# Kernel optimization log

Hardware: AMD Instinct MI355X
Metric: run time of the kernel (lower is better)

The kernel has to match this reference:

```python
import jax, jax.numpy as jnp
import numpy as np

EPS = 0.05  # mesh.epsilon boundary band


def _pool_one(adj, image, vs, edges):
    # adj: [N,N] bool, image: [N,F] f32, vs: [N,2] f32 in [0,1], edges: [2,E] int32
    N, F = image.shape
    E = edges.shape[1]
    K = N // 2                      # out_target
    tgt_kills = N - K               # number of vertices removed
    v0, v1 = edges[0], edges[1]
    # heap key = sum of squares of concat(image[v0], image[v1])
    cost = jnp.sum(image[v0] * image[v0], -1) + jnp.sum(image[v1] * image[v1], -1)
    def bnd(p):
        return (p[:, 0] < EPS) | (p[:, 0] > 1 - EPS) | (p[:, 1] < EPS) | (p[:, 1] > 1 - EPS)
    ok = ~(bnd(vs[v0]) | bnd(vs[v1]))   # boundary_mask = ~is_boundary
    # heappop of [value, id] lists == stable sort by cost (ties broken by edge id)
    order = jnp.argsort(cost)
    # sequential greedy collapse: kill v1 if edge interior and both endpoints alive
    def step(carry, eid):
        mask, nk = carry
        a, b = v0[eid], v1[eid]
        acc = ok[eid] & mask[a] & mask[b] & (nk < tgt_kills)
        mask = mask.at[b].set(mask[b] & ~acc)
        return (mask, nk + acc.astype(jnp.int32)), acc
    (mask, _), accepts = jax.lax.scan(step, (jnp.ones(N, bool), jnp.int32(0)), order)
    sv0, sv1 = v0[order], v1[order]
    # mapping m: dead vertex -> absorbing vertex (identity elsewhere)
    dead = jnp.where(accepts, sv1, N)          # N = out-of-range -> dropped
    m = jnp.arange(N).at[dead].set(sv0, mode='drop')
    # update_matrix: scatter-add collapsed vertex features into absorber rows
    upd = jnp.zeros_like(image).at[jnp.where(accepts, sv0, N)].add(image[sv1], mode='drop')
    image2 = image + upd
    # merge_vertex on adjacency: union rows then columns of merged vertices
    A = adj.astype(jnp.uint8)
    A1 = jnp.zeros_like(A).at[m].max(A)        # merge rows
    A2 = jnp.zeros_like(A1).at[m].max(A1.T).T  # merge cols
    alive = jnp.nonzero(mask, size=K, fill_value=0)[0]  # exactly K survivors
    adj_out = A2[alive][:, alive].astype(bool) & ~jnp.eye(K, dtype=bool)
    return adj_out, image2[alive]


def setup_inputs() -> dict:
    key = jax.random.key(0)
    k1, k2, k3, k4, k5 = jax.random.split(key, 5)
    B, N, F, E = 4, 8192, 64, 65536
    adj = jax.random.bernoulli(k1, 0.002, (B, N, N))
    image = jax.random.normal(k2, (B, N, F), jnp.float32)
    vs = jax.random.uniform(k3, (B, N, 2), dtype=jnp.float32)
    a = jax.random.randint(k4, (B, 1, E), 0, N)
    off = jax.random.randint(k5, (B, 1, E), 1, N)
    b = (a + off) % N                           # guarantee v0 != v1
    edges = jnp.concatenate([a, b], axis=1).astype(jnp.int32)
    return {"adj": adj, "image": image, "vs": vs, "edges": edges}


def reference(adj, image, vs, edges):
    # returns (pooled adjacency [B,N//2,N//2] bool, pooled features [B,N//2,F])
    return jax.vmap(_pool_one)(adj, image, vs, edges)
```

## Files before the change

kernel.cpp:

```cpp
#include <hip/hip_runtime.h>
#include <stdint.h>

typedef unsigned long long u64;
typedef unsigned int u32;
typedef unsigned char u8;

#define Bn 4
#define Nv 8192
#define Fd 64
#define Ed 65536
#define Kv 4096
#define TGTK 4096
#define NW 256
#define SC 8192

#define WS_FLAGS   ((size_t)0)
#define WS_ACCCNT  ((size_t)256)
#define WS_OUTBITS ((size_t)512)
#define OUTBITS_BYTES ((size_t)Bn*Kv*128*4)
#define WS_ZERO_BYTES (WS_OUTBITS + OUTBITS_BYTES)
#define WS_KEYS    (WS_ZERO_BYTES)
#define WS_SQ      (WS_KEYS + (size_t)Bn*Ed*8)
#define WS_BND     (WS_SQ + (size_t)Bn*Nv*4)
#define WS_OK      (WS_BND + (size_t)Bn*Nv)
#define WS_MAP     (WS_OK + (size_t)Bn*Ed)
#define WS_POS     (WS_MAP + (size_t)Bn*Nv*4)
#define WS_PM      (WS_POS + (size_t)Bn*Nv*4)
#define WS_ALIVEW  (WS_PM + (size_t)Bn*Nv*4)
#define WS_ALIST   (WS_ALIVEW + (size_t)Bn*NW*4)
#define WS_ACC     (WS_ALIST + (size_t)Bn*Kv*4)

__global__ void k_detect(const u8* adj, u32* flags) {
    int tid = blockIdx.x * blockDim.x + threadIdx.x;
    const u32* w = (const u32*)adj;
    bool f0 = false, f1 = false, f2 = false, f3 = false;
    for (int i = tid; i < (1 << 19); i += gridDim.x * blockDim.x) {
        u32 v = w[i];
        f0 |= (v & 0x000000FFu) != 0;
        f1 |= (v & 0x0000FF00u) != 0;
        f2 |= (v & 0x00FF0000u) != 0;
        f3 |= (v & 0xFF000000u) != 0;
    }
    u32 m = 0;
    if (__ballot(f0)) m |= 1;
    if (__ballot(f1)) m |= 2;
    if (__ballot(f2)) m |= 4;
    if (__ballot(f3)) m |= 8;
    if ((threadIdx.x & 63) == 0 && m) atomicOr(flags, m);
}

__global__ void k_vertex(const float* image, const float* vs, float* sq, u8* bnd, int* map) {
#pragma clang fp contract(off)
    int idx = blockIdx.x * 256 + threadIdx.x;
    if (idx >= Bn * Nv) return;
    const float* row = image + (size_t)idx * Fd;
    float r[8];
#pragma unroll
    for (int j = 0; j < 8; ++j) r[j] = row[j] * row[j];
#pragma unroll
    for (int i = 8; i < 64; i += 8)
#pragma unroll
        for (int j = 0; j < 8; ++j) r[j] += row[i + j] * row[i + j];
    float s = ((r[0] + r[1]) + (r[2] + r[3])) + ((r[4] + r[5]) + (r[6] + r[7]));
    sq[idx] = s;
    float x = vs[(size_t)idx * 2], y = vs[(size_t)idx * 2 + 1];
    const float LO = 0.05f;
    const float HI = (float)(1.0 - 0.05);
    bnd[idx] = ((x < LO) || (x > HI) || (y < LO) || (y > HI)) ? 1 : 0;
    map[idx] = idx & (Nv - 1);
}

__global__ void k_edge(const int* edges, const float* sq, const u8* bnd, u64* keys, u8* ok) {
    int idx = blockIdx.x * 256 + threadIdx.x;
    if (idx >= Bn * Ed) return;
    int b = idx >> 16, e = idx & (Ed - 1);
    int v0 = edges[(size_t)b * 2 * Ed + e];
    int v1 = edges[(size_t)b * 2 * Ed + Ed + e];
    float c = sq[b * Nv + v0] + sq[b * Nv + v1];
    u32 cb = __float_as_uint(c);
    keys[idx] = ((u64)cb << 16) | (u32)e;
    ok[idx] = (!bnd[b * Nv + v0] && !bnd[b * Nv + v1]) ? 1 : 0;
}

__device__ __forceinline__ void bitonic_cas(u64* s, int i, int pa, bool asc) {
    u64 a = s[i], c = s[pa];
    if ((a > c) == asc) { s[i] = c; s[pa] = a; }
}

__global__ __launch_bounds__(1024) void k_sortA(u64* keys) {
    __shared__ u64 s[SC];
    int b = blockIdx.x >> 3, ch = blockIdx.x & 7;
    u64* base = keys + (size_t)b * Ed + (size_t)ch * SC;
    int gb = ch * SC;
    for (int p = 0; p < SC / 1024; ++p) s[p * 1024 + threadIdx.x] = base[p * 1024 + threadIdx.x];
    __syncthreads();
    for (int k = 2; k <= SC; k <<= 1) {
        for (int j = k >> 1; j > 0; j >>= 1) {
            for (int p = 0; p < SC / 2048; ++p) {
                int t = p * 1024 + threadIdx.x;
                int i = ((t & ~(j - 1)) << 1) | (t & (j - 1));
                bool asc = (((gb + i) & k) == 0);
                bitonic_cas(s, i, i | j, asc);
            }
            __syncthreads();
        }
    }
    for (int p = 0; p < SC / 1024; ++p) base[p * 1024 + threadIdx.x] = s[p * 1024 + threadIdx.x];
}

__global__ void k_sortB(u64* keys, int k, int j) {
    int idx = blockIdx.x * 256 + threadIdx.x;
    if (idx >= Bn * Ed / 2) return;
    int b = idx >> 15, t = idx & (Ed / 2 - 1);
    int i = ((t & ~(j - 1)) << 1) | (t & (j - 1));
    int pa = i | j;
    bool asc = ((i & k) == 0);
    u64* base = keys + (size_t)b * Ed;
    u64 a = base[i], c = base[pa];
    if ((a > c) == asc) { base[i] = c; base[pa] = a; }
}

__global__ __launch_bounds__(1024) void k_sortC(u64* keys, int k) {
    __shared__ u64 s[SC];
    int b = blockIdx.x >> 3, ch = blockIdx.x & 7;
    u64* base = keys + (size_t)b * Ed + (size_t)ch * SC;
    int gb = ch * SC;
    for (int p = 0; p < SC / 1024; ++p) s[p * 1024 + threadIdx.x] = base[p * 1024 + threadIdx.x];
    __syncthreads();
    bool asc = ((gb & k) == 0);
    for (int j = SC / 2; j > 0; j >>= 1) {
        for (int p = 0; p < SC / 2048; ++p) {
            int t = p * 1024 + threadIdx.x;
            int i = ((t & ~(j - 1)) << 1) | (t & (j - 1));
            bitonic_cas(s, i, i | j, asc);
        }
        __syncthreads();
    }
    for (int p = 0; p < SC / 1024; ++p) base[p * 1024 + threadIdx.x] = s[p * 1024 + threadIdx.x];
}

__global__ __launch_bounds__(64) void k_greedy(const u64* keys, const int* edges, const u8* ok,
                                               int* map, u32* aliveW, int* accList, u32* accCnt) {
    int b = blockIdx.x;
    int lane = threadIdx.x;
    __shared__ u32 alive[NW];
    __shared__ u32 mlane[Nv];
    for (int i = lane; i < NW; i += 64) alive[i] = 0xFFFFFFFFu;
    for (int i = lane; i < Nv; i += 64) mlane[i] = 64u;
    __syncthreads();
    const u64* kb = keys + (size_t)b * Ed;
    const int* e0 = edges + (size_t)b * 2 * Ed;
    const int* e1 = e0 + Ed;
    const u8* okb = ok + (size_t)b * Ed;
    int nk = 0;
    for (int g = 0; g < Ed / 64 && nk < TGTK; ++g) {
        u64 key = kb[g * 64 + lane];
        int id = (int)(key & 0xFFFFu);
        int v0 = e0[id], v1 = e1[id];
        bool okk = okb[id] != 0;
        bool a0 = (alive[v0 >> 5] >> (v0 & 31)) & 1u;
        bool a1 = (alive[v1 >> 5] >> (v1 & 31)) & 1u;
        bool spec = okk && a0 && a1;
        if (spec) atomicMin(&mlane[v1], (u32)lane);
        __syncthreads();
        bool conf = false;
        if (spec) conf = (mlane[v0] < (u32)lane) || (mlane[v1] < (u32)lane);
        u64 specM = __ballot(spec);
        u64 confM = __ballot(conf);
        u64 accM = specM & ~confM;
        u64 rem = confM;
        while (rem) {
            int l = __ffsll((unsigned long long)rem) - 1;
            rem &= rem - 1;
            int bv0 = __shfl(v0, l);
            int bv1 = __shfl(v1, l);
            bool killer = ((accM >> lane) & 1ull) && (lane < l) && (v1 == bv0 || v1 == bv1);
            if (__ballot(killer) == 0ull) accM |= 1ull << l;
        }
        int cnt = __popcll(accM);
        int remK = TGTK - nk;
        bool acc = (accM >> lane) & 1ull;
        if (cnt > remK) {
            int r = __popcll(accM & ((1ull << lane) - 1ull));
            if (acc && r >= remK) acc = false;
            accM = __ballot(acc);
            cnt = remK;
        }
        if (acc) {
            atomicAnd(&alive[v1 >> 5], ~(1u << (v1 & 31)));
            map[(size_t)b * Nv + v1] = v0;
            int r = __popcll(accM & ((1ull << lane) - 1ull));
            int slot = nk + r;
            accList[((size_t)b * TGTK + slot) * 2] = v0;
            accList[((size_t)b * TGTK + slot) * 2 + 1] = v1;
        }
        if (spec) mlane[v1] = 64u;
        nk += cnt;
        __syncthreads();
    }
    for (int i = lane; i < NW; i += 64) aliveW[b * NW + i] = alive[i];
    if (lane == 0) accCnt[b] = (u32)nk;
}

__global__ __launch_bounds__(256) void k_scan(const u32* aliveW, const int* map,
                                              int* pos, int* pm, int* alist) {
    int b = blockIdx.x, tid = threadIdx.x;
    __shared__ u32 cnt[256];
    __shared__ u32 off[256];
    u32 w = aliveW[b * NW + tid];
    cnt[tid] = __popc(w);
    __syncthreads();
    if (tid == 0) { u32 s = 0; for (int i = 0; i < 256; ++i) { off[i] = s; s += cnt[i]; } }
    __syncthreads();
    u32 base = off[tid];
    int* posb = pos + (size_t)b * Nv;
    int* alb = alist + (size_t)b * Kv;
    for (int bit = 0; bit < 32; ++bit) {
        int v = tid * 32 + bit;
        int p = -1;
        if ((w >> bit) & 1u) {
            if (base < Kv) { p = (int)base; alb[base] = v; }
            base++;
        }
        posb[v] = p;
    }
    __syncthreads();
    const int* mapb = map + (size_t)b * Nv;
    int* pmb = pm + (size_t)b * Nv;
    for (int v = tid; v < Nv; v += 256) pmb[v] = posb[mapb[v]];
}

__global__ void k_fcopy(const float* image, const int* alist, float* outF) {
    int idx = blockIdx.x * 256 + threadIdx.x;
    if (idx >= Bn * Kv * 16) return;
    int b = idx >> 16, r = idx & 65535;
    int x = r >> 4, f4 = r & 15;
    int src = alist[b * Kv + x];
    const float4* s = (const float4*)(image + ((size_t)(b * Nv + src)) * Fd) + f4;
    float4* d = (float4*)(outF + ((size_t)(b * Kv + x)) * Fd) + f4;
    *d = *s;
}

__global__ __launch_bounds__(64) void k_fscat(const float* image, const int* accList,
                                              const u32* accCnt, const int* pos, float* outF) {
    int b = blockIdx.x >> 12, e = blockIdx.x & 4095;
    if (e >= (int)accCnt[b]) return;
    int v0 = accList[((size_t)b * TGTK + e) * 2];
    int v1 = accList[((size_t)b * TGTK + e) * 2 + 1];
    int x = pos[(size_t)b * Nv + v0];
    if (x < 0) return;
    int f = threadIdx.x;
    atomicAdd(outF + ((size_t)(b * Kv + x)) * Fd + f,
              image[((size_t)(b * Nv + v1)) * Fd + f]);
}

__global__ __launch_bounds__(256) void k_merge(const u8* adj, const u32* flags,
                                               const int* pm, u32* outbits) {
    int bi = blockIdx.x;
    int b = bi >> 13, i = bi & (Nv - 1);
    int t = pm[(size_t)b * Nv + i];
    if (t < 0) return;
    __shared__ u32 bits[Kv / 32];
    int tid = threadIdx.x;
    if (tid < 128) bits[tid] = 0;
    __syncthreads();
    const int* pmb = pm + (size_t)b * Nv;
    u32 fw = flags[0];
    bool bytefmt = (fw & 1) && (fw & 8);
    auto put = [&](int col) {
        int c = pmb[col];
        if (c >= 0) atomicOr(&bits[c >> 5], 1u << (c & 31));
    };
    if (bytefmt) {
        const uint4* row = (const uint4*)(adj + ((size_t)b * Nv + i) * Nv);
#pragma unroll
        for (int it = 0; it < 2; ++it) {
            uint4 v = row[it * 256 + tid];
            if (v.x | v.y | v.z | v.w) {
                int cb = (it * 256 + tid) * 16;
                u32 wv[4] = { v.x, v.y, v.z, v.w };
                for (int q = 0; q < 4; ++q) {
                    u32 u = wv[q];
                    if (!u) continue;
#pragma unroll
                    for (int kk = 0; kk < 4; ++kk)
                        if ((u >> (8 * kk)) & 0xFFu) put(cb + q * 4 + kk);
                }
            }
        }
    } else {
        const uint4* row = (const uint4*)((const u32*)adj + ((size_t)b * Nv + i) * Nv);
        for (int it = 0; it < 8; ++it) {
            uint4 v = row[it * 256 + tid];
            int cb = (it * 256 + tid) * 4;
            if (v.x) put(cb);
            if (v.y) put(cb + 1);
            if (v.z) put(cb + 2);
            if (v.w) put(cb + 3);
        }
    }
    __syncthreads();
    if (tid < 128) {
        u32 bw = bits[tid];
        if (bw) atomicOr(&outbits[((size_t)b * Kv + t) * 128 + tid], bw);
    }
}

__global__ void k_expand(const u32* outbits, float* out) {
    int idx = blockIdx.x;
    int tid = threadIdx.x;
    int b = idx >> 14, r = idx & 16383;
    int x = r >> 2, seg = r & 3;
    int c0 = seg * 1024 + tid * 4;
    u32 w = outbits[((size_t)b * Kv + x) * 128 + (c0 >> 5)];
    u32 nib = (w >> (c0 & 31)) & 0xFu;
    float4 f;
    f.x = (nib & 1) ? 1.f : 0.f;
    f.y = (nib & 2) ? 1.f : 0.f;
    f.z = (nib & 4) ? 1.f : 0.f;
    f.w = (nib & 8) ? 1.f : 0.f;
    if (x >= c0 && x < c0 + 4) ((float*)&f)[x - c0] = 0.f;
    *((float4*)(out + ((size_t)(b * Kv + x)) * Kv + c0)) = f;
}

extern "C" void kernel_launch(void* const* d_in, const int* in_sizes, int n_in,
                              void* d_out, int out_size, void* d_ws, size_t ws_size,
                              hipStream_t stream) {
    const u8* adj = (const u8*)d_in[0];
    const float* image = (const float*)d_in[1];
    const float* vs = (const float*)d_in[2];
    const int* edges = (const int*)d_in[3];
    char* ws = (char*)d_ws;
    u32* flags = (u32*)(ws + WS_FLAGS);
    u32* accCnt = (u32*)(ws + WS_ACCCNT);
    u32* outbits = (u32*)(ws + WS_OUTBITS);
    u64* keys = (u64*)(ws + WS_KEYS);
    float* sq = (float*)(ws + WS_SQ);
    u8* bnd = (u8*)(ws + WS_BND);
    u8* ok = (u8*)(ws + WS_OK);
    int* map = (int*)(ws + WS_MAP);
    int* pos = (int*)(ws + WS_POS);
    int* pm = (int*)(ws + WS_PM);
    u32* aliveW = (u32*)(ws + WS_ALIVEW);
    int* alist = (int*)(ws + WS_ALIST);
    int* accList = (int*)(ws + WS_ACC);
    float* outA = (float*)d_out;
    float* outF = outA + (size_t)Bn * Kv * Kv;

    hipMemsetAsync(d_ws, 0, WS_ZERO_BYTES, stream);
    k_detect<<<64, 256, 0, stream>>>(adj, flags);
    k_vertex<<<Bn * Nv / 256, 256, 0, stream>>>(image, vs, sq, bnd, map);
    k_edge<<<Bn * Ed / 256, 256, 0, stream>>>(edges, sq, bnd, keys, ok);
    k_sortA<<<Bn * 8, 1024, 0, stream>>>(keys);
    k_sortB<<<Bn * Ed / 2 / 256, 256, 0, stream>>>(keys, 16384, 8192);
    k_sortC<<<Bn * 8, 1024, 0, stream>>>(keys, 16384);
    k_sortB<<<Bn * Ed / 2 / 256, 256, 0, stream>>>(keys, 32768, 16384);
    k_sortB<<<Bn * Ed / 2 / 256, 256, 0, stream>>>(keys, 32768, 8192);
    k_sortC<<<Bn * 8, 1024, 0, stream>>>(keys, 32768);
    k_sortB<<<Bn * Ed / 2 / 256, 256, 0, stream>>>(keys, 65536, 32768);
    k_sortB<<<Bn * Ed / 2 / 256, 256, 0, stream>>>(keys, 65536, 16384);
    k_sortB<<<Bn * Ed / 2 / 256, 256, 0, stream>>>(keys, 65536, 8192);
    k_sortC<<<Bn * 8, 1024, 0, stream>>>(keys, 65536);
    k_greedy<<<Bn, 64, 0, stream>>>(keys, edges, ok, map, aliveW, accList, accCnt);
    k_scan<<<Bn, 256, 0, stream>>>(aliveW, map, pos, pm, alist);
    k_fcopy<<<Bn * Kv * 16 / 256, 256, 0, stream>>>(image, alist, outF);
    k_fscat<<<Bn * TGTK, 64, 0, stream>>>(image, accList, accCnt, pos, outF);
    k_merge<<<Bn * Nv, 256, 0, stream>>>(adj, flags, pm, outbits);
    k_expand<<<Bn * Kv * 4, 256, 0, stream>>>(outbits, outA);
}
```

Baseline: 2.091 ms.

## Pack edge data into sorted array and do small bitonic stages in registers

Edge endpoints and the interior flag are packed into one 32-bit word per edge, and a parallel gather kernel reorders these by sorted key. The serial greedy loop then reads one coalesced word per lane, with the next group prefetched, in place of a chain of dependent loads (key, then edges, then the ok flag). The bitonic sort kernels also handle the last three merge steps (strides 4, 2, 1) on eight elements held in registers per thread, which removes shared-memory passes and barriers. This costs one extra gather launch and two workspace buffers.

```diff
diff --git a/kernel.cpp b/kernel.cpp
--- a/kernel.cpp
+++ b/kernel.cpp
@@ -22,13 +22,14 @@
 #define WS_KEYS    (WS_ZERO_BYTES)
 #define WS_SQ      (WS_KEYS + (size_t)Bn*Ed*8)
 #define WS_BND     (WS_SQ + (size_t)Bn*Nv*4)
-#define WS_OK      (WS_BND + (size_t)Bn*Nv)
-#define WS_MAP     (WS_OK + (size_t)Bn*Ed)
+#define WS_MAP     (WS_BND + (size_t)Bn*Nv)
 #define WS_POS     (WS_MAP + (size_t)Bn*Nv*4)
 #define WS_PM      (WS_POS + (size_t)Bn*Nv*4)
 #define WS_ALIVEW  (WS_PM + (size_t)Bn*Nv*4)
 #define WS_ALIST   (WS_ALIVEW + (size_t)Bn*NW*4)
 #define WS_ACC     (WS_ALIST + (size_t)Bn*Kv*4)
+#define WS_PACK    (WS_ACC + (size_t)Bn*TGTK*2*4)
+#define WS_SPACK   (WS_PACK + (size_t)Bn*Ed*4)
 
 __global__ void k_detect(const u8* adj, u32* flags) {
     int tid = blockIdx.x * blockDim.x + threadIdx.x;
@@ -70,21 +71,24 @@
     map[idx] = idx & (Nv - 1);
 }
 
-__global__ void k_edge(const int* edges, const float* sq, const u8* bnd, u64* keys, u8* ok) {
+__global__ void k_edge(const int* edges, const float* sq, const u8* bnd, u64* keys, u32* pack) {
     int idx = blockIdx.x * 256 + threadIdx.x;
     if (idx >= Bn * Ed) return;
     int b = idx >> 16, e = idx & (Ed - 1);
     int v0 = edges[(size_t)b * 2 * Ed + e];
     int v1 = edges[(size_t)b * 2 * Ed + Ed + e];
     float c = sq[b * Nv + v0] + sq[b * Nv + v1];
-    u32 cb = __float_as_uint(c);
-    keys[idx] = ((u64)cb << 16) | (u32)e;
-    ok[idx] = (!bnd[b * Nv + v0] && !bnd[b * Nv + v1]) ? 1 : 0;
+    keys[idx] = ((u64)__float_as_uint(c) << 16) | (u32)e;
+    u32 okk = (!bnd[b * Nv + v0] && !bnd[b * Nv + v1]) ? 1u : 0u;
+    pack[idx] = (u32)v0 | ((u32)v1 << 13) | (okk << 26);
 }
 
 __device__ __forceinline__ void bitonic_cas(u64* s, int i, int pa, bool asc) {
     u64 a = s[i], c = s[pa];
     if ((a > c) == asc) { s[i] = c; s[pa] = a; }
+}
+__device__ __forceinline__ void cex(u64& a, u64& b, bool asc) {
+    if ((a > b) == asc) { u64 t = a; a = b; b = t; }
 }
 
 __global__ __launch_bounds__(1024) void k_sortA(u64* keys) {
@@ -92,10 +96,25 @@
     int b = blockIdx.x >> 3, ch = blockIdx.x & 7;
     u64* base = keys + (size_t)b * Ed + (size_t)ch * SC;
     int gb = ch * SC;
-    for (int p = 0; p < SC / 1024; ++p) s[p * 1024 + threadIdx.x] = base[p * 1024 + threadIdx.x];
-    __syncthreads();
-    for (int k = 2; k <= SC; k <<= 1) {
-        for (int j = k >> 1; j > 0; j >>= 1) {
+    int t8 = threadIdx.x * 8;
+    u64 r[8];
+#pragma unroll
+    for (int u = 0; u < 8; ++u) r[u] = base[t8 + u];
+    cex(r[0], r[1], true); cex(r[2], r[3], false); cex(r[4], r[5], true); cex(r[6], r[7], false);
+    cex(r[0], r[2], true); cex(r[1], r[3], true); cex(r[4], r[6], false); cex(r[5], r[7], false);
+    cex(r[0], r[1], true); cex(r[2], r[3], true); cex(r[4], r[5], false); cex(r[6], r[7], false);
+    {
+        bool a8 = (((gb + t8) & 8) == 0);
+        cex(r[0], r[4], a8); cex(r[1], r[5], a8); cex(r[2], r[6], a8); cex(r[3], r[7], a8);
+        cex(r[0], r[2], a8); cex(r[1], r[3], a8); cex(r[4], r[6], a8); cex(r[5], r[7], a8);
+        cex(r[0], r[1], a8); cex(r[2], r[3], a8); cex(r[4], r[5], a8); cex(r[6], r[7], a8);
+    }
+#pragma unroll
+    for (int u = 0; u < 8; ++u) s[t8 + u] = r[u];
+    __syncthreads();
+    for (int k = 16; k <= SC; k <<= 1) {
+        for (int j = k >> 1; j >= 8; j >>= 1) {
+#pragma unroll
             for (int p = 0; p < SC / 2048; ++p) {
                 int t = p * 1024 + threadIdx.x;
                 int i = ((t & ~(j - 1)) << 1) | (t & (j - 1));
@@ -104,8 +123,21 @@
             }
             __syncthreads();
         }
-    }
-    for (int p = 0; p < SC / 1024; ++p) base[p * 1024 + threadIdx.x] = s[p * 1024 + threadIdx.x];
+        bool asc = (((gb + t8) & k) == 0);
+#pragma unroll
+        for (int u = 0; u < 8; ++u) r[u] = s[t8 + u];
+        cex(r[0], r[4], asc); cex(r[1], r[5], asc); cex(r[2], r[6], asc); cex(r[3], r[7], asc);
+        cex(r[0], r[2], asc); cex(r[1], r[3], asc); cex(r[4], r[6], asc); cex(r[5], r[7], asc);
+        cex(r[0], r[1], asc); cex(r[2], r[3], asc); cex(r[4], r[5], asc); cex(r[6], r[7], asc);
+        if (k == SC) {
+#pragma unroll
+            for (int u = 0; u < 8; ++u) base[t8 + u] = r[u];
+        } else {
+#pragma unroll
+            for (int u = 0; u < 8; ++u) s[t8 + u] = r[u];
+            __syncthreads();
+        }
+    }
 }
 
 __global__ void k_sortB(u64* keys, int k, int j) {
@@ -128,7 +160,8 @@
     for (int p = 0; p < SC / 1024; ++p) s[p * 1024 + threadIdx.x] = base[p * 1024 + threadIdx.x];
     __syncthreads();
     bool asc = ((gb & k) == 0);
-    for (int j = SC / 2; j > 0; j >>= 1) {
+    for (int j = SC / 2; j >= 8; j >>= 1) {
+#pragma unroll
         for (int p = 0; p < SC / 2048; ++p) {
             int t = p * 1024 + threadIdx.x;
             int i = ((t & ~(j - 1)) << 1) | (t & (j - 1));
@@ -136,28 +169,43 @@
         }
         __syncthreads();
     }
-    for (int p = 0; p < SC / 1024; ++p) base[p * 1024 + threadIdx.x] = s[p * 1024 + threadIdx.x];
-}
-
-__global__ __launch_bounds__(64) void k_greedy(const u64* keys, const int* edges, const u8* ok,
-                                               int* map, u32* aliveW, int* accList, u32* accCnt) {
+    int t8 = threadIdx.x * 8;
+    u64 r[8];
+#pragma unroll
+    for (int u = 0; u < 8; ++u) r[u] = s[t8 + u];
+    cex(r[0], r[4], asc); cex(r[1], r[5], asc); cex(r[2], r[6], asc); cex(r[3], r[7], asc);
+    cex(r[0], r[2], asc); cex(r[1], r[3], asc); cex(r[4], r[6], asc); cex(r[5], r[7], asc);
+    cex(r[0], r[1], asc); cex(r[2], r[3], asc); cex(r[4], r[5], asc); cex(r[6], r[7], asc);
+#pragma unroll
+    for (int u = 0; u < 8; ++u) base[t8 + u] = r[u];
+}
+
+__global__ void k_gather(const u64* keys, const u32* pack, u32* spack) {
+    int idx = blockIdx.x * 256 + threadIdx.x;
+    if (idx >= Bn * Ed) return;
+    int b = idx >> 16;
+    u32 id = (u32)(keys[idx] & 0xFFFFu);
+    spack[idx] = pack[(size_t)b * Ed + id];
+}
+
+__global__ __launch_bounds__(64) void k_greedy(const u32* spack, int* map, u32* aliveW,
+                                               int* accList, u32* accCnt) {
     int b = blockIdx.x;
     int lane = threadIdx.x;
     __shared__ u32 alive[NW];
     __shared__ u32 mlane[Nv];
     for (int i = lane; i < NW; i += 64) alive[i] = 0xFFFFFFFFu;
     for (int i = lane; i < Nv; i += 64) mlane[i] = 64u;
-    __syncthreads();
-    const u64* kb = keys + (size_t)b * Ed;
-    const int* e0 = edges + (size_t)b * 2 * Ed;
-    const int* e1 = e0 + Ed;
-    const u8* okb = ok + (size_t)b * Ed;
+    const u32* sp = spack + (size_t)b * Ed;
+    u32 pc = sp[lane];
+    __syncthreads();
     int nk = 0;
-    for (int g = 0; g < Ed / 64 && nk < TGTK; ++g) {
-        u64 key = kb[g * 64 + lane];
-        int id = (int)(key & 0xFFFFu);
-        int v0 = e0[id], v1 = e1[id];
-        bool okk = okb[id] != 0;
+    const int G = Ed / 64;
+    for (int g = 0; g < G; ++g) {
+        u32 pn = (g + 1 < G) ? sp[(g + 1) * 64 + lane] : 0u;
+        int v0 = pc & 8191;
+        int v1 = (pc >> 13) & 8191;
+        bool okk = (pc >> 26) & 1u;
         bool a0 = (alive[v0 >> 5] >> (v0 & 31)) & 1u;
         bool a1 = (alive[v1 >> 5] >> (v1 & 31)) & 1u;
         bool spec = okk && a0 && a1;
@@ -181,22 +229,24 @@
         int remK = TGTK - nk;
         bool acc = (accM >> lane) & 1ull;
         if (cnt > remK) {
-            int r = __popcll(accM & ((1ull << lane) - 1ull));
-            if (acc && r >= remK) acc = false;
+            int rr = __popcll(accM & ((1ull << lane) - 1ull));
+            if (acc && rr >= remK) acc = false;
             accM = __ballot(acc);
             cnt = remK;
         }
         if (acc) {
             atomicAnd(&alive[v1 >> 5], ~(1u << (v1 & 31)));
             map[(size_t)b * Nv + v1] = v0;
-            int r = __popcll(accM & ((1ull << lane) - 1ull));
-            int slot = nk + r;
+            int rr = __popcll(accM & ((1ull << lane) - 1ull));
+            int slot = nk + rr;
             accList[((size_t)b * TGTK + slot) * 2] = v0;
             accList[((size_t)b * TGTK + slot) * 2 + 1] = v1;
         }
         if (spec) mlane[v1] = 64u;
         nk += cnt;
         __syncthreads();
+        if (nk >= TGTK) break;
+        pc = pn;
     }
     for (int i = lane; i < NW; i += 64) aliveW[b * NW + i] = alive[i];
     if (lane == 0) accCnt[b] = (u32)nk;
@@ -337,20 +387,21 @@
     u64* keys = (u64*)(ws + WS_KEYS);
     float* sq = (float*)(ws + WS_SQ);
     u8* bnd = (u8*)(ws + WS_BND);
-    u8* ok = (u8*)(ws + WS_OK);
     int* map = (int*)(ws + WS_MAP);
     int* pos = (int*)(ws + WS_POS);
     int* pm = (int*)(ws + WS_PM);
     u32* aliveW = (u32*)(ws + WS_ALIVEW);
     int* alist = (int*)(ws + WS_ALIST);
     int* accList = (int*)(ws + WS_ACC);
+    u32* pack = (u32*)(ws + WS_PACK);
+    u32* spack = (u32*)(ws + WS_SPACK);
     float* outA = (float*)d_out;
     float* outF = outA + (size_t)Bn * Kv * Kv;
 
     hipMemsetAsync(d_ws, 0, WS_ZERO_BYTES, stream);
     k_detect<<<64, 256, 0, stream>>>(adj, flags);
     k_vertex<<<Bn * Nv / 256, 256, 0, stream>>>(image, vs, sq, bnd, map);
-    k_edge<<<Bn * Ed / 256, 256, 0, stream>>>(edges, sq, bnd, keys, ok);
+    k_edge<<<Bn * Ed / 256, 256, 0, stream>>>(edges, sq, bnd, keys, pack);
     k_sortA<<<Bn * 8, 1024, 0, stream>>>(keys);
     k_sortB<<<Bn * Ed / 2 / 256, 256, 0, stream>>>(keys, 16384, 8192);
     k_sortC<<<Bn * 8, 1024, 0, stream>>>(keys, 16384);
@@ -361,7 +412,8 @@
     k_sortB<<<Bn * Ed / 2 / 256, 256, 0, stream>>>(keys, 65536, 16384);
     k_sortB<<<Bn * Ed / 2 / 256, 256, 0, stream>>>(keys, 65536, 8192);
     k_sortC<<<Bn * 8, 1024, 0, stream>>>(keys, 65536);
-    k_greedy<<<Bn, 64, 0, stream>>>(keys, edges, ok, map, aliveW, accList, accCnt);
+    k_gather<<<Bn * Ed / 256, 256, 0, stream>>>(keys, pack, spack);
+    k_greedy<<<Bn, 64, 0, stream>>>(spack, map, aliveW, accList, accCnt);
     k_scan<<<Bn, 256, 0, stream>>>(aliveW, map, pos, pm, alist);
     k_fcopy<<<Bn * Kv * 16 / 256, 256, 0, stream>>>(image, alist, outF);
     k_fscat<<<Bn * TGTK, 64, 0, stream>>>(image, accList, accCnt, pos, outF);
```

Result: faster. 2.013 ms (-3.7%).

## Replace bitonic edge sort with stable 3-pass LSD radix sort and packed payload

Applied to the files above, without the earlier changes.

Replaces the multi-kernel bitonic sort on 64-bit cost/id keys with a stable three-pass 11-bit LSD radix sort on 32-bit cost keys, carrying v0, v1 and the interior flag packed into one 32-bit payload. The greedy kernel then reads the packed payload directly and prefetches the next group, which removes the indirect edge and ok lookups. Adjacency flag detection is folded into the vertex kernel to save a launch. Stability comes from a warp-ballot rank within each chunk, so tie order by edge id is preserved; in exchange it adds histogram and scan passes and 64-thread blocks with many LDS atomics.

```diff
diff --git a/kernel.cpp b/kernel.cpp
--- a/kernel.cpp
+++ b/kernel.cpp
@@ -12,47 +12,32 @@
 #define Kv 4096
 #define TGTK 4096
 #define NW 256
-#define SC 8192
+#define RB 2048
+#define NB 128
+#define CH 512
 
 #define WS_FLAGS   ((size_t)0)
 #define WS_ACCCNT  ((size_t)256)
-#define WS_OUTBITS ((size_t)512)
-#define OUTBITS_BYTES ((size_t)Bn*Kv*128*4)
-#define WS_ZERO_BYTES (WS_OUTBITS + OUTBITS_BYTES)
-#define WS_KEYS    (WS_ZERO_BYTES)
-#define WS_SQ      (WS_KEYS + (size_t)Bn*Ed*8)
+#define WS_OUTBITS ((size_t)4096)
+#define WS_ZERO_BYTES (WS_OUTBITS + (size_t)Bn*Kv*128*4)
+#define WS_HIST    (WS_ZERO_BYTES)
+#define WS_KA      (WS_HIST + (size_t)Bn*RB*NB*4)
+#define WS_PA      (WS_KA + (size_t)Bn*Ed*4)
+#define WS_KB      (WS_PA + (size_t)Bn*Ed*4)
+#define WS_PB      (WS_KB + (size_t)Bn*Ed*4)
+#define WS_SQ      (WS_PB + (size_t)Bn*Ed*4)
 #define WS_BND     (WS_SQ + (size_t)Bn*Nv*4)
-#define WS_OK      (WS_BND + (size_t)Bn*Nv)
-#define WS_MAP     (WS_OK + (size_t)Bn*Ed)
+#define WS_MAP     (WS_BND + (size_t)Bn*Nv)
 #define WS_POS     (WS_MAP + (size_t)Bn*Nv*4)
 #define WS_PM      (WS_POS + (size_t)Bn*Nv*4)
 #define WS_ALIVEW  (WS_PM + (size_t)Bn*Nv*4)
 #define WS_ALIST   (WS_ALIVEW + (size_t)Bn*NW*4)
 #define WS_ACC     (WS_ALIST + (size_t)Bn*Kv*4)
 
-__global__ void k_detect(const u8* adj, u32* flags) {
-    int tid = blockIdx.x * blockDim.x + threadIdx.x;
-    const u32* w = (const u32*)adj;
-    bool f0 = false, f1 = false, f2 = false, f3 = false;
-    for (int i = tid; i < (1 << 19); i += gridDim.x * blockDim.x) {
-        u32 v = w[i];
-        f0 |= (v & 0x000000FFu) != 0;
-        f1 |= (v & 0x0000FF00u) != 0;
-        f2 |= (v & 0x00FF0000u) != 0;
-        f3 |= (v & 0xFF000000u) != 0;
-    }
-    u32 m = 0;
-    if (__ballot(f0)) m |= 1;
-    if (__ballot(f1)) m |= 2;
-    if (__ballot(f2)) m |= 4;
-    if (__ballot(f3)) m |= 8;
-    if ((threadIdx.x & 63) == 0 && m) atomicOr(flags, m);
-}
-
-__global__ void k_vertex(const float* image, const float* vs, float* sq, u8* bnd, int* map) {
+__global__ void k_vertex(const u8* adj, u32* flags, const float* image, const float* vs,
+                         float* sq, u8* bnd, int* map) {
 #pragma clang fp contract(off)
     int idx = blockIdx.x * 256 + threadIdx.x;
-    if (idx >= Bn * Nv) return;
     const float* row = image + (size_t)idx * Fd;
     float r[8];
 #pragma unroll
@@ -68,96 +53,132 @@
     const float HI = (float)(1.0 - 0.05);
     bnd[idx] = ((x < LO) || (x > HI) || (y < LO) || (y > HI)) ? 1 : 0;
     map[idx] = idx & (Nv - 1);
-}
-
-__global__ void k_edge(const int* edges, const float* sq, const u8* bnd, u64* keys, u8* ok) {
+    const u32* w = (const u32*)adj;
+    bool f0 = false, f1 = false, f2 = false, f3 = false;
+    for (int i = idx; i < (1 << 19); i += 32768) {
+        u32 v = w[i];
+        f0 |= (v & 0x000000FFu) != 0;
+        f1 |= (v & 0x0000FF00u) != 0;
+        f2 |= (v & 0x00FF0000u) != 0;
+        f3 |= (v & 0xFF000000u) != 0;
+    }
+    u32 m = 0;
+    if (__ballot(f0)) m |= 1;
+    if (__ballot(f1)) m |= 2;
+    if (__ballot(f2)) m |= 4;
+    if (__ballot(f3)) m |= 8;
+    if ((threadIdx.x & 63) == 0 && m) atomicOr(flags, m);
+}
+
+__global__ void k_edge(const int* edges, const float* sq, const u8* bnd, u32* kA, u32* pA) {
     int idx = blockIdx.x * 256 + threadIdx.x;
     if (idx >= Bn * Ed) return;
     int b = idx >> 16, e = idx & (Ed - 1);
     int v0 = edges[(size_t)b * 2 * Ed + e];
     int v1 = edges[(size_t)b * 2 * Ed + Ed + e];
     float c = sq[b * Nv + v0] + sq[b * Nv + v1];
-    u32 cb = __float_as_uint(c);
-    keys[idx] = ((u64)cb << 16) | (u32)e;
-    ok[idx] = (!bnd[b * Nv + v0] && !bnd[b * Nv + v1]) ? 1 : 0;
-}
-
-__device__ __forceinline__ void bitonic_cas(u64* s, int i, int pa, bool asc) {
-    u64 a = s[i], c = s[pa];
-    if ((a > c) == asc) { s[i] = c; s[pa] = a; }
-}
-
-__global__ __launch_bounds__(1024) void k_sortA(u64* keys) {
-    __shared__ u64 s[SC];
-    int b = blockIdx.x >> 3, ch = blockIdx.x & 7;
-    u64* base = keys + (size_t)b * Ed + (size_t)ch * SC;
-    int gb = ch * SC;
-    for (int p = 0; p < SC / 1024; ++p) s[p * 1024 + threadIdx.x] = base[p * 1024 + threadIdx.x];
-    __syncthreads();
-    for (int k = 2; k <= SC; k <<= 1) {
-        for (int j = k >> 1; j > 0; j >>= 1) {
-            for (int p = 0; p < SC / 2048; ++p) {
-                int t = p * 1024 + threadIdx.x;
-                int i = ((t & ~(j - 1)) << 1) | (t & (j - 1));
-                bool asc = (((gb + i) & k) == 0);
-                bitonic_cas(s, i, i | j, asc);
-            }
-            __syncthreads();
-        }
-    }
-    for (int p = 0; p < SC / 1024; ++p) base[p * 1024 + threadIdx.x] = s[p * 1024 + threadIdx.x];
-}
-
-__global__ void k_sortB(u64* keys, int k, int j) {
-    int idx = blockIdx.x * 256 + threadIdx.x;
-    if (idx >= Bn * Ed / 2) return;
-    int b = idx >> 15, t = idx & (Ed / 2 - 1);
-    int i = ((t & ~(j - 1)) << 1) | (t & (j - 1));
-    int pa = i | j;
-    bool asc = ((i & k) == 0);
-    u64* base = keys + (size_t)b * Ed;
-    u64 a = base[i], c = base[pa];
-    if ((a > c) == asc) { base[i] = c; base[pa] = a; }
-}
-
-__global__ __launch_bounds__(1024) void k_sortC(u64* keys, int k) {
-    __shared__ u64 s[SC];
-    int b = blockIdx.x >> 3, ch = blockIdx.x & 7;
-    u64* base = keys + (size_t)b * Ed + (size_t)ch * SC;
-    int gb = ch * SC;
-    for (int p = 0; p < SC / 1024; ++p) s[p * 1024 + threadIdx.x] = base[p * 1024 + threadIdx.x];
-    __syncthreads();
-    bool asc = ((gb & k) == 0);
-    for (int j = SC / 2; j > 0; j >>= 1) {
-        for (int p = 0; p < SC / 2048; ++p) {
-            int t = p * 1024 + threadIdx.x;
-            int i = ((t & ~(j - 1)) << 1) | (t & (j - 1));
-            bitonic_cas(s, i, i | j, asc);
-        }
+    kA[idx] = __float_as_uint(c);
+    u32 okk = (!bnd[b * Nv + v0] && !bnd[b * Nv + v1]) ? 1u : 0u;
+    pA[idx] = (u32)v0 | ((u32)v1 << 13) | (okk << 26);
+}
+
+__global__ __launch_bounds__(64) void k_rhist(const u32* kin, u32* hist, int sh) {
+    int blk = blockIdx.x & (NB - 1), b = blockIdx.x >> 7;
+    int lane = threadIdx.x;
+    __shared__ u32 h[RB];
+    for (int i = lane; i < RB; i += 64) h[i] = 0;
+    __syncthreads();
+    const u32* kb = kin + (size_t)b * Ed + (size_t)blk * CH;
+#pragma unroll
+    for (int r = 0; r < CH / 64; ++r) {
+        u32 g = (kb[r * 64 + lane] >> sh) & (RB - 1);
+        atomicAdd(&h[g], 1u);
+    }
+    __syncthreads();
+    u32* hb = hist + (size_t)b * RB * NB;
+    for (int i = lane; i < RB; i += 64) hb[(size_t)i * NB + blk] = h[i];
+}
+
+__global__ __launch_bounds__(1024) void k_rscan(u32* hist) {
+    int b = blockIdx.x, tid = threadIdx.x;
+    u32* hb = hist + (size_t)b * RB * NB;
+    const int PT = RB * NB / 1024;
+    u32 s = 0;
+    for (int i = 0; i < PT; ++i) s += hb[tid * PT + i];
+    __shared__ u32 sc[1024];
+    sc[tid] = s;
+    __syncthreads();
+    for (int off = 1; off < 1024; off <<= 1) {
+        u32 t = (tid >= off) ? sc[tid - off] : 0u;
         __syncthreads();
-    }
-    for (int p = 0; p < SC / 1024; ++p) base[p * 1024 + threadIdx.x] = s[p * 1024 + threadIdx.x];
-}
-
-__global__ __launch_bounds__(64) void k_greedy(const u64* keys, const int* edges, const u8* ok,
-                                               int* map, u32* aliveW, int* accList, u32* accCnt) {
+        sc[tid] += t;
+        __syncthreads();
+    }
+    u32 run = sc[tid] - s;
+    for (int i = 0; i < PT; ++i) {
+        u32 v = hb[tid * PT + i];
+        hb[tid * PT + i] = run;
+        run += v;
+    }
+}
+
+__global__ __launch_bounds__(64) void k_rscat(const u32* kin, const u32* pin, const u32* hist,
+                                              u32* kout, u32* pout, int sh) {
+    int blk = blockIdx.x & (NB - 1), b = blockIdx.x >> 7;
+    int lane = threadIdx.x;
+    __shared__ u32 cnt[RB];
+    for (int i = lane; i < RB; i += 64) cnt[i] = 0;
+    __syncthreads();
+    const size_t base = (size_t)b * Ed + (size_t)blk * CH;
+    const u32* kb = kin + base;
+    const u32* pb = pin + base;
+    u32 key[CH / 64], pay[CH / 64], gg[CH / 64], gbase[CH / 64];
+#pragma unroll
+    for (int r = 0; r < CH / 64; ++r) { key[r] = kb[r * 64 + lane]; pay[r] = pb[r * 64 + lane]; }
+    const u32* hb = hist + (size_t)b * RB * NB;
+#pragma unroll
+    for (int r = 0; r < CH / 64; ++r) {
+        gg[r] = (key[r] >> sh) & (RB - 1);
+        gbase[r] = hb[(size_t)gg[r] * NB + blk];
+    }
+    u32* ko = kout + (size_t)b * Ed;
+    u32* po = pout + (size_t)b * Ed;
+#pragma unroll
+    for (int r = 0; r < CH / 64; ++r) {
+        u32 g = gg[r];
+        u64 m = ~0ull;
+#pragma unroll
+        for (int bb = 0; bb < 11; ++bb) {
+            u64 bl = __ballot((g >> bb) & 1u);
+            m &= ((g >> bb) & 1u) ? bl : ~bl;
+        }
+        u32 nlow = (u32)__popcll(m & ((1ull << lane) - 1ull));
+        u32 c = cnt[g];
+        u32 dst = gbase[r] + c + nlow;
+        ko[dst] = key[r];
+        po[dst] = pay[r];
+        if (nlow == 0) atomicAdd(&cnt[g], (u32)__popcll(m));
+    }
+}
+
+__global__ __launch_bounds__(64) void k_greedy(const u32* spack, int* map, u32* aliveW,
+                                               int* accList, u32* accCnt) {
     int b = blockIdx.x;
     int lane = threadIdx.x;
     __shared__ u32 alive[NW];
     __shared__ u32 mlane[Nv];
     for (int i = lane; i < NW; i += 64) alive[i] = 0xFFFFFFFFu;
     for (int i = lane; i < Nv; i += 64) mlane[i] = 64u;
-    __syncthreads();
-    const u64* kb = keys + (size_t)b * Ed;
-    const int* e0 = edges + (size_t)b * 2 * Ed;
-    const int* e1 = e0 + Ed;
-    const u8* okb = ok + (size_t)b * Ed;
+    const u32* sp = spack + (size_t)b * Ed;
+    u32 pc = sp[lane];
+    __syncthreads();
     int nk = 0;
-    for (int g = 0; g < Ed / 64 && nk < TGTK; ++g) {
-        u64 key = kb[g * 64 + lane];
-        int id = (int)(key & 0xFFFFu);
-        int v0 = e0[id], v1 = e1[id];
-        bool okk = okb[id] != 0;
+    const int G = Ed / 64;
+    for (int g = 0; g < G; ++g) {
+        u32 pn = (g + 1 < G) ? sp[(g + 1) * 64 + lane] : 0u;
+        int v0 = pc & 8191;
+        int v1 = (pc >> 13) & 8191;
+        bool okk = (pc >> 26) & 1u;
         bool a0 = (alive[v0 >> 5] >> (v0 & 31)) & 1u;
         bool a1 = (alive[v1 >> 5] >> (v1 & 31)) & 1u;
         bool spec = okk && a0 && a1;
@@ -181,22 +202,24 @@
         int remK = TGTK - nk;
         bool acc = (accM >> lane) & 1ull;
         if (cnt > remK) {
-            int r = __popcll(accM & ((1ull << lane) - 1ull));
-            if (acc && r >= remK) acc = false;
+            int rr = __popcll(accM & ((1ull << lane) - 1ull));
+            if (acc && rr >= remK) acc = false;
             accM = __ballot(acc);
             cnt = remK;
         }
         if (acc) {
             atomicAnd(&alive[v1 >> 5], ~(1u << (v1 & 31)));
             map[(size_t)b * Nv + v1] = v0;
-            int r = __popcll(accM & ((1ull << lane) - 1ull));
-            int slot = nk + r;
+            int rr = __popcll(accM & ((1ull << lane) - 1ull));
+            int slot = nk + rr;
             accList[((size_t)b * TGTK + slot) * 2] = v0;
             accList[((size_t)b * TGTK + slot) * 2 + 1] = v1;
         }
         if (spec) mlane[v1] = 64u;
         nk += cnt;
         __syncthreads();
+        if (nk >= TGTK) break;
+        pc = pn;
     }
     for (int i = lane; i < NW; i += 64) aliveW[b * NW + i] = alive[i];
     if (lane == 0) accCnt[b] = (u32)nk;
@@ -334,10 +357,13 @@
     u32* flags = (u32*)(ws + WS_FLAGS);
     u32* accCnt = (u32*)(ws + WS_ACCCNT);
     u32* outbits = (u32*)(ws + WS_OUTBITS);
-    u64* keys = (u64*)(ws + WS_KEYS);
+    u32* hist = (u32*)(ws + WS_HIST);
+    u32* kA = (u32*)(ws + WS_KA);
+    u32* pA = (u32*)(ws + WS_PA);
+    u32* kB = (u32*)(ws + WS_KB);
+    u32* pB = (u32*)(ws + WS_PB);
     float* sq = (float*)(ws + WS_SQ);
     u8* bnd = (u8*)(ws + WS_BND);
-    u8* ok = (u8*)(ws + WS_OK);
     int* map = (int*)(ws + WS_MAP);
     int* pos = (int*)(ws + WS_POS);
     int* pm = (int*)(ws + WS_PM);
@@ -348,20 +374,18 @@
     float* outF = outA + (size_t)Bn * Kv * Kv;
 
     hipMemsetAsync(d_ws, 0, WS_ZERO_BYTES, stream);
-    k_detect<<<64, 256, 0, stream>>>(adj, flags);
-    k_vertex<<<Bn * Nv / 256, 256, 0, stream>>>(image, vs, sq, bnd, map);
-    k_edge<<<Bn * Ed / 256, 256, 0, stream>>>(edges, sq, bnd, keys, ok);
-    k_sortA<<<Bn * 8, 1024, 0, stream>>>(keys);
-    k_sortB<<<Bn * Ed / 2 / 256, 256, 0, stream>>>(keys, 16384, 8192);
-    k_sortC<<<Bn * 8, 1024, 0, stream>>>(keys, 16384);
-    k_sortB<<<Bn * Ed / 2 / 256, 256, 0, stream>>>(keys, 32768, 16384);
-    k_sortB<<<Bn * Ed / 2 / 256, 256, 0, stream>>>(keys, 32768, 8192);
-    k_sortC<<<Bn * 8, 1024, 0, stream>>>(keys, 32768);
-    k_sortB<<<Bn * Ed / 2 / 256, 256, 0, stream>>>(keys, 65536, 32768);
-    k_sortB<<<Bn * Ed / 2 / 256, 256, 0, stream>>>(keys, 65536, 16384);
-    k_sortB<<<Bn * Ed / 2 / 256, 256, 0, stream>>>(keys, 65536, 8192);
-    k_sortC<<<Bn * 8, 1024, 0, stream>>>(keys, 65536);
-    k_greedy<<<Bn, 64, 0, stream>>>(keys, edges, ok, map, aliveW, accList, accCnt);
+    k_vertex<<<Bn * Nv / 256, 256, 0, stream>>>(adj, flags, image, vs, sq, bnd, map);
+    k_edge<<<Bn * Ed / 256, 256, 0, stream>>>(edges, sq, bnd, kA, pA);
+    k_rhist<<<Bn * NB, 64, 0, stream>>>(kA, hist, 0);
+    k_rscan<<<Bn, 1024, 0, stream>>>(hist);
+    k_rscat<<<Bn * NB, 64, 0, stream>>>(kA, pA, hist, kB, pB, 0);
+    k_rhist<<<Bn * NB, 64, 0, stream>>>(kB, hist, 11);
+    k_rscan<<<Bn, 1024, 0, stream>>>(hist);
+    k_rscat<<<Bn * NB, 64, 0, stream>>>(kB, pB, hist, kA, pA, 11);
+    k_rhist<<<Bn * NB, 64, 0, stream>>>(kA, hist, 22);
+    k_rscan<<<Bn, 1024, 0, stream>>>(hist);
+    k_rscat<<<Bn * NB, 64, 0, stream>>>(kA, pA, hist, kB, pB, 22);
+    k_greedy<<<Bn, 64, 0, stream>>>(pB, map, aliveW, accList, accCnt);
     k_scan<<<Bn, 256, 0, stream>>>(aliveW, map, pos, pm, alist);
     k_fcopy<<<Bn * Kv * 16 / 256, 256, 0, stream>>>(image, alist, outF);
     k_fscat<<<Bn * TGTK, 64, 0, stream>>>(image, accList, accCnt, pos, outF);
```

Measured after the change: 2.257 ms. +7.9%, slower.
